# Kernel optimization log

Measured on AMD Instinct MI355X. Metric: run time of the kernel, lower is better.

The kernel has to match this reference:

```python
import jax, jax.numpy as jnp
import numpy as np

D_IN, D_K, D_V = 768, 128, 768


def setup_inputs() -> dict:
    key = jax.random.key(0)
    ks = jax.random.split(key, 7)
    x = jax.random.normal(ks[0], (4, 2048, D_IN), dtype=jnp.float32)
    s_in = 1.0 / np.sqrt(D_IN)
    Wq = jax.random.uniform(ks[1], (D_IN, D_K), minval=-s_in, maxval=s_in, dtype=jnp.float32)
    bq = jax.random.uniform(ks[2], (D_K,), minval=-s_in, maxval=s_in, dtype=jnp.float32)
    Wk = jax.random.uniform(ks[3], (D_IN, D_K), minval=-s_in, maxval=s_in, dtype=jnp.float32)
    bk = jax.random.uniform(ks[4], (D_K,), minval=-s_in, maxval=s_in, dtype=jnp.float32)
    Wv = jax.random.uniform(ks[5], (D_IN, D_V), minval=-s_in, maxval=s_in, dtype=jnp.float32)
    bv = jax.random.uniform(ks[6], (D_V,), minval=-s_in, maxval=s_in, dtype=jnp.float32)
    return {"x": x, "Wq": Wq, "bq": bq, "Wk": Wk, "bk": bk, "Wv": Wv, "bv": bv}


def reference(x, Wq, bq, Wk, bk, Wv, bv):
    # q,k: [b,t,d_k]; v: [b,t,d_v]
    q = jnp.einsum('bti,ik->btk', x, Wq) + bq
    k = jnp.einsum('bti,ik->btk', x, Wk) + bk
    v = jnp.einsum('bti,iv->btv', x, Wv) + bv
    scale = 1.0 / jnp.sqrt(jnp.asarray(D_K, dtype=jnp.float32))
    scores = jnp.einsum('bqk,btk->bqt', q, k) * scale  # [b,t,t]
    attn = jax.nn.softmax(scores, axis=-1)
    return jnp.einsum('bqt,btv->bqv', attn, v)
```

## Files before the change

### kernel.cpp

```cpp
#include <hip/hip_runtime.h>
#include <stdint.h>

typedef unsigned short u16;
typedef __attribute__((ext_vector_type(8))) short short8;
typedef __attribute__((ext_vector_type(4))) float f32x4;

#define BATCH 4
#define SEQ   2048
#define DIN   768
#define DK    128
#define DV    768
#define MTOT  (BATCH*SEQ)
#define NQKV  1024

__device__ __forceinline__ u16 f2bf(float f) {
  union { float f; uint32_t u; } v; v.f = f;
  uint32_t r = v.u + 0x7FFFu + ((v.u >> 16) & 1u);
  return (u16)(r >> 16);
}
__device__ __forceinline__ float bf2f(u16 h) {
  union { uint32_t u; float f; } v; v.u = ((uint32_t)h) << 16;
  return v.f;
}

template<int N> __device__ __forceinline__ void wait_vmcnt() {
  if constexpr (N == 0) asm volatile("s_waitcnt vmcnt(0)" ::: "memory");
  else if constexpr (N == 5) asm volatile("s_waitcnt vmcnt(5)" ::: "memory");
  else if constexpr (N == 10) asm volatile("s_waitcnt vmcnt(10)" ::: "memory");
}

__global__ __launch_bounds__(256) void pack_all(
    const float* __restrict__ Wq, const float* __restrict__ bq,
    const float* __restrict__ Wk, const float* __restrict__ bk,
    const float* __restrict__ Wv, const float* __restrict__ bv,
    u16* __restrict__ WbT, float* __restrict__ biasP) {
  const float qs = 0.088388347648318447f;
  __shared__ u16 tile[64][72];
  int y = blockIdx.y;
  const float* W; u16* dst; int ldw, nb; float sc;
  if (y < 2)      { W = Wq; dst = WbT;                       ldw = DK; sc = qs;   nb = y;     }
  else if (y < 4) { W = Wk; dst = WbT + (size_t)DK * DIN;    ldw = DK; sc = 1.0f; nb = y - 2; }
  else            { W = Wv; dst = WbT + (size_t)2*DK * DIN;  ldw = DV; sc = 1.0f; nb = y - 4; }
  int i0 = blockIdx.x * 64;
  int n0 = nb * 64;
  int tid = threadIdx.x;
  if (blockIdx.x == 0 && y == 0) {
    for (int n = tid; n < NQKV; n += 256)
      biasP[n] = (n < DK) ? bq[n] * qs : (n < 2*DK ? bk[n - DK] : bv[n - 2*DK]);
  }
  int tr = tid >> 2;
  int tc = (tid & 3) * 16;
  const float* src = W + (size_t)(i0 + tr) * ldw + n0 + tc;
  u16 o[16];
#pragma unroll
  for (int u = 0; u < 16; u += 4) {
    float4 v = *(const float4*)(src + u);
    o[u] = f2bf(v.x * sc); o[u+1] = f2bf(v.y * sc); o[u+2] = f2bf(v.z * sc); o[u+3] = f2bf(v.w * sc);
  }
  *(uint4*)&tile[tr][tc]     = *(const uint4*)&o[0];
  *(uint4*)&tile[tr][tc + 8] = *(const uint4*)&o[8];
  __syncthreads();
  u16 tmp[16];
#pragma unroll
  for (int u = 0; u < 16; ++u) tmp[u] = tile[tc + u][tr];
  u16* d = dst + (size_t)(n0 + tr) * DIN + i0 + tc;
  *(uint4*)d       = *(const uint4*)&tmp[0];
  *(uint4*)(d + 8) = *(const uint4*)&tmp[8];
}

__global__ void convert_x(const float* __restrict__ x, u16* __restrict__ xb) {
  int i = (blockIdx.x * blockDim.x + threadIdx.x) * 4;
  float4 v = *(const float4*)(x + i);
  u16 o[4] = { f2bf(v.x), f2bf(v.y), f2bf(v.z), f2bf(v.w) };
  *(uint2*)(xb + i) = *(const uint2*)o;
}

__global__ __launch_bounds__(512, 4) void gemm_proj(
    const u16* __restrict__ A, const u16* __restrict__ BT,
    u16* __restrict__ C0, u16* __restrict__ C1,
    const float* __restrict__ bias)
{
  const int NJ = 2, CH = 4, gx = 64;
  __shared__ u16 As[2][128][64];
  __shared__ u16 Bs[2][NJ * 64][64];
  const int tid = threadIdx.x;
  const int l   = tid & 63;
  const int wid = tid >> 6;
  const int wm  = wid >> 2;
  const int wn  = wid & 3;

  const int nwg = gridDim.x;
  const int cpx = nwg >> 3;
  const int bid = blockIdx.x;
  const int wg  = (bid & 7) * cpx + (bid >> 3);
  const int by  = wg / gx;
  const int bx  = wg - by * gx;
  const int m0  = bx * 128;
  const int n0  = by * (NJ * 64);

  f32x4 acc[4][NJ] = {};
  const int lr = l >> 3;
  const int lc = ((l & 7) ^ lr) * 8;
  const int ca = wid * CH;

  auto STAGE = [&](int buf, int k0) {
#pragma unroll
    for (int i = 0; i < CH; ++i) {
      int c = ca + i;
      if (c < 16) {
        const u16* src = A + (size_t)(m0 + c * 8 + lr) * DIN + k0 + lc;
        __builtin_amdgcn_global_load_lds(
            (const __attribute__((address_space(1))) unsigned int*)src,
            (__attribute__((address_space(3))) unsigned int*)&As[buf][c * 8][0],
            16, 0, 0);
      } else {
        int cb = c - 16;
        const u16* src = BT + (size_t)(n0 + cb * 8 + lr) * DIN + k0 + lc;
        __builtin_amdgcn_global_load_lds(
            (const __attribute__((address_space(1))) unsigned int*)src,
            (__attribute__((address_space(3))) unsigned int*)&Bs[buf][cb * 8][0],
            16, 0, 0);
      }
    }
  };

  STAGE(0, 0);
  __syncthreads();
  int cur = 0;
  for (int k0 = 0; k0 < DIN; k0 += 64) {
    if (k0 + 64 < DIN) STAGE(cur ^ 1, k0 + 64);
#pragma unroll
    for (int ks = 0; ks < 2; ++ks) {
      short8 af[4], bg[NJ];
#pragma unroll
      for (int i = 0; i < 4; ++i) {
        int row  = wm * 64 + i * 16 + (l & 15);
        int slot = (ks * 4 + (l >> 4)) ^ (row & 7);
        af[i] = *(const short8*)&As[cur][row][slot * 8];
      }
#pragma unroll
      for (int j = 0; j < NJ; ++j) {
        int row  = wn * (NJ * 16) + j * 16 + (l & 15);
        int slot = (ks * 4 + (l >> 4)) ^ (row & 7);
        bg[j] = *(const short8*)&Bs[cur][row][slot * 8];
      }
#pragma unroll
      for (int i = 0; i < 4; ++i)
#pragma unroll
        for (int j = 0; j < NJ; ++j)
          acc[i][j] = __builtin_amdgcn_mfma_f32_16x16x32_bf16(af[i], bg[j], acc[i][j], 0, 0, 0);
    }
    __syncthreads();
    cur ^= 1;
  }

  const int rbase = (l >> 4) * 4;
  const int cl    = l & 15;
#pragma unroll
  for (int i = 0; i < 4; ++i) {
#pragma unroll
    for (int j = 0; j < NJ; ++j) {
      int col = n0 + wn * (NJ * 16) + j * 16 + cl;
      int row0 = m0 + wm * 64 + i * 16 + rbase;
      float bv_ = bias[col];
      if (n0 < 256) {
#pragma unroll
        for (int q = 0; q < 4; ++q)
          C0[(size_t)(row0 + q) * 256 + col] = f2bf(acc[i][j][q] + bv_);
      } else {
        int b = row0 >> 11, t = row0 & 2047;
        u16 o[4];
#pragma unroll
        for (int q = 0; q < 4; ++q) o[q] = f2bf(acc[i][j][q] + bv_);
        *(uint2*)&C1[((size_t)b * DV + (col - 256)) * SEQ + t] = *(const uint2*)o;
      }
    }
  }
}

__global__ __launch_bounds__(512, 2) void gemm_pv(
    const u16* __restrict__ P, const u16* __restrict__ vT,
    float* __restrict__ out)
{
  const int NJ = 3, CH = 5, gx = 16, gy = 4, NT = SEQ / 64;
  __shared__ u16 As[3][128][64];
  __shared__ u16 Bs[3][NJ * 64][64];
  const int tid = threadIdx.x;
  const int l   = tid & 63;
  const int wid = tid >> 6;
  const int wm  = wid >> 2;
  const int wn  = wid & 3;

  const int nwg = gridDim.x;
  const int cpx = nwg >> 3;
  const int bid = blockIdx.x;
  const int wg  = (bid & 7) * cpx + (bid >> 3);
  const int z   = wg / (gx * gy);
  const int rem = wg - z * gx * gy;
  const int by  = rem / gx;
  const int bx  = rem - by * gx;
  const int m0  = bx * 128;
  const int n0  = by * (NJ * 64);

  const u16* A  = P  + (size_t)z * SEQ * SEQ;
  const u16* BT = vT + (size_t)z * DV * SEQ;

  f32x4 acc[4][NJ] = {};
  f32x4 accO[4] = {};
  const short8 kOnes = {16256,16256,16256,16256,16256,16256,16256,16256};

  const int lr = l >> 3;
  const int lc = ((l & 7) ^ lr) * 8;
  const int ca = wid * CH;

  auto STAGE = [&](int buf, int k0) {
#pragma unroll
    for (int i = 0; i < CH; ++i) {
      int c = ca + i;
      if (c < 16) {
        const u16* src = A + (size_t)(m0 + c * 8 + lr) * SEQ + k0 + lc;
        __builtin_amdgcn_global_load_lds(
            (const __attribute__((address_space(1))) unsigned int*)src,
            (__attribute__((address_space(3))) unsigned int*)&As[buf][c * 8][0],
            16, 0, 0);
      } else {
        int cb = c - 16;
        const u16* src = BT + (size_t)(n0 + cb * 8 + lr) * SEQ + k0 + lc;
        __builtin_amdgcn_global_load_lds(
            (const __attribute__((address_space(1))) unsigned int*)src,
            (__attribute__((address_space(3))) unsigned int*)&Bs[buf][cb * 8][0],
            16, 0, 0);
      }
    }
  };

  auto COMPUTE = [&](int buf) {
#pragma unroll
    for (int ks = 0; ks < 2; ++ks) {
      short8 af[4], bg[NJ];
#pragma unroll
      for (int i = 0; i < 4; ++i) {
        int row  = wm * 64 + i * 16 + (l & 15);
        int slot = (ks * 4 + (l >> 4)) ^ (row & 7);
        af[i] = *(const short8*)&As[buf][row][slot * 8];
      }
#pragma unroll
      for (int j = 0; j < NJ; ++j) {
        int row  = wn * (NJ * 16) + j * 16 + (l & 15);
        int slot = (ks * 4 + (l >> 4)) ^ (row & 7);
        bg[j] = *(const short8*)&Bs[buf][row][slot * 8];
      }
#pragma unroll
      for (int i = 0; i < 4; ++i)
#pragma unroll
        for (int j = 0; j < NJ; ++j)
          acc[i][j] = __builtin_amdgcn_mfma_f32_16x16x32_bf16(af[i], bg[j], acc[i][j], 0, 0, 0);
#pragma unroll
      for (int i = 0; i < 4; ++i)
        accO[i] = __builtin_amdgcn_mfma_f32_16x16x32_bf16(af[i], kOnes, accO[i], 0, 0, 0);
    }
  };

  STAGE(0, 0);
  STAGE(1, 64);
  int cur = 0;
  for (int t = 0; t < NT - 1; ++t) {
    wait_vmcnt<CH>();
    __builtin_amdgcn_s_barrier();
    COMPUTE(cur);
    if (t + 2 < NT) STAGE(cur + 2 >= 3 ? cur - 1 : cur + 2, (t + 2) * 64);
    cur = (cur + 1 == 3) ? 0 : cur + 1;
  }
  wait_vmcnt<0>();
  __builtin_amdgcn_s_barrier();
  COMPUTE(cur);

  const int rbase = (l >> 4) * 4;
  const int cl    = l & 15;
#pragma unroll
  for (int i = 0; i < 4; ++i) {
    f32x4 rs;
#pragma unroll
    for (int q = 0; q < 4; ++q) rs[q] = 1.0f / accO[i][q];
#pragma unroll
    for (int j = 0; j < NJ; ++j) {
      int col  = n0 + wn * (NJ * 16) + j * 16 + cl;
      int row0 = m0 + wm * 64 + i * 16 + rbase;
#pragma unroll
      for (int q = 0; q < 4; ++q)
        out[(size_t)z * SEQ * DV + (size_t)(row0 + q) * DV + col] = acc[i][j][q] * rs[q];
    }
  }
}

__global__ __launch_bounds__(512, 4) void sgemm_exp(
    const u16* __restrict__ qk, u16* __restrict__ P)
{
  __shared__ u16 As[128][128];
  __shared__ u16 Bs[128][128];
  const int tid = threadIdx.x;
  const int l   = tid & 63;
  const int wid = tid >> 6;
  const int wm  = wid >> 2;
  const int wn  = wid & 3;

  const int nwg = gridDim.x;
  const int cpx = nwg >> 3;
  const int bid = blockIdx.x;
  const int wg  = (bid & 7) * cpx + (bid >> 3);
  const int z   = wg >> 8;
  const int rem = wg & 255;
  const int by  = rem >> 4;
  const int bx  = rem & 15;
  const int m0  = bx * 128;
  const int n0  = by * 128;

  const u16* A  = qk + (size_t)z * SEQ * 256;
  const u16* BT = qk + DK + (size_t)z * SEQ * 256;

  const int rin  = l >> 4;
  const int s16  = l & 15;
#pragma unroll
  for (int i = 0; i < 8; ++i) {
    int c = wid * 8 + i;
    if (c < 32) {
      int r = c * 4 + rin;
      int gs = s16 ^ (r & 7);
      const u16* src = A + (size_t)(m0 + r) * 256 + gs * 8;
      __builtin_amdgcn_global_load_lds(
          (const __attribute__((address_space(1))) unsigned int*)src,
          (__attribute__((address_space(3))) unsigned int*)&As[c * 4][0],
          16, 0, 0);
    } else {
      int cb = c - 32;
      int r = cb * 4 + rin;
      int gs = s16 ^ (r & 7);
      const u16* src = BT + (size_t)(n0 + r) * 256 + gs * 8;
      __builtin_amdgcn_global_load_lds(
          (const __attribute__((address_space(1))) unsigned int*)src,
          (__attribute__((address_space(3))) unsigned int*)&Bs[cb * 4][0],
          16, 0, 0);
    }
  }
  __syncthreads();

  f32x4 acc[4][2] = {};
#pragma unroll
  for (int ks = 0; ks < 4; ++ks) {
    short8 af[4], bg[2];
#pragma unroll
    for (int i = 0; i < 4; ++i) {
      int row  = wm * 64 + i * 16 + (l & 15);
      int slot = (ks * 4 + (l >> 4)) ^ (row & 7);
      af[i] = *(const short8*)&As[row][slot * 8];
    }
#pragma unroll
    for (int j = 0; j < 2; ++j) {
      int row  = wn * 32 + j * 16 + (l & 15);
      int slot = (ks * 4 + (l >> 4)) ^ (row & 7);
      bg[j] = *(const short8*)&Bs[row][slot * 8];
    }
#pragma unroll
    for (int i = 0; i < 4; ++i)
#pragma unroll
      for (int j = 0; j < 2; ++j)
        acc[i][j] = __builtin_amdgcn_mfma_f32_16x16x32_bf16(af[i], bg[j], acc[i][j], 0, 0, 0);
  }

  const int rbase = (l >> 4) * 4;
  const int cl    = l & 15;
  u16* Pz = P + (size_t)z * SEQ * SEQ;
#pragma unroll
  for (int i = 0; i < 4; ++i)
#pragma unroll
    for (int j = 0; j < 2; ++j) {
      int col  = n0 + wn * 32 + j * 16 + cl;
      int row0 = m0 + wm * 64 + i * 16 + rbase;
#pragma unroll
      for (int q = 0; q < 4; ++q)
        Pz[(size_t)(row0 + q) * SEQ + col] = f2bf(__expf(acc[i][j][q]));
    }
}

extern "C" void kernel_launch(void* const* d_in, const int* in_sizes, int n_in,
                              void* d_out, int out_size, void* d_ws, size_t ws_size,
                              hipStream_t stream) {
  const float* x  = (const float*)d_in[0];
  const float* Wq = (const float*)d_in[1];
  const float* bq = (const float*)d_in[2];
  const float* Wk = (const float*)d_in[3];
  const float* bk = (const float*)d_in[4];
  const float* Wv = (const float*)d_in[5];
  const float* bv = (const float*)d_in[6];
  float* out = (float*)d_out;

  size_t off = 0;
  auto alloc = [&](size_t bytes) -> void* {
    void* p = (char*)d_ws + off;
    off += (bytes + 255) & ~(size_t)255;
    return p;
  };
  u16*   xb    = (u16*)alloc((size_t)MTOT * DIN * 2);
  u16*   WbT   = (u16*)alloc((size_t)NQKV * DIN * 2);
  float* biasP = (float*)alloc(NQKV * 4);
  u16*   qk    = (u16*)alloc((size_t)MTOT * 256 * 2);
  u16*   vT    = (u16*)alloc((size_t)BATCH * DV * SEQ * 2);
  u16*   P     = (u16*)alloc((size_t)BATCH * SEQ * SEQ * 2);
  if (off > ws_size) return;

  pack_all<<<dim3(DIN/64, 16), dim3(256), 0, stream>>>(Wq, bq, Wk, bk, Wv, bv, WbT, biasP);
  convert_x<<<dim3((MTOT * DIN / 4) / 256), dim3(256), 0, stream>>>(x, xb);

  gemm_proj<<<dim3(64 * 8), dim3(512), 0, stream>>>(xb, WbT, qk, vT, biasP);

  sgemm_exp<<<dim3(16 * 16 * BATCH), dim3(512), 0, stream>>>(qk, P);

  gemm_pv<<<dim3(16 * 4 * BATCH), dim3(512), 0, stream>>>(P, vT, out);
}
```

Measured before the change: 85.52 us.

## Merge prep kernels and interleave prefetch with MFMA in PV gemm

Combines the weight-packing and x-conversion kernels into one launch, removing one kernel launch and its gap. In the PV gemm, the global-to-LDS prefetch for tile t+2 is split across the two k-substeps and issued before the MFMAs, with s_setprio raised around the MFMA block, so loads overlap compute instead of following it. The loop is also unified so the last iteration needs no separate tail. It adds branching in the staging loop and changes instruction scheduling, which the compiler may not handle well.

```diff
diff --git a/kernel.cpp b/kernel.cpp
--- a/kernel.cpp
+++ b/kernel.cpp
@@ -18,10 +18,6 @@
   uint32_t r = v.u + 0x7FFFu + ((v.u >> 16) & 1u);
   return (u16)(r >> 16);
 }
-__device__ __forceinline__ float bf2f(u16 h) {
-  union { uint32_t u; float f; } v; v.u = ((uint32_t)h) << 16;
-  return v.f;
-}
 
 template<int N> __device__ __forceinline__ void wait_vmcnt() {
   if constexpr (N == 0) asm volatile("s_waitcnt vmcnt(0)" ::: "memory");
@@ -29,22 +25,32 @@
   else if constexpr (N == 10) asm volatile("s_waitcnt vmcnt(10)" ::: "memory");
 }
 
-__global__ __launch_bounds__(256) void pack_all(
+__global__ __launch_bounds__(256) void prep(
+    const float* __restrict__ x, u16* __restrict__ xb,
     const float* __restrict__ Wq, const float* __restrict__ bq,
     const float* __restrict__ Wk, const float* __restrict__ bk,
     const float* __restrict__ Wv, const float* __restrict__ bv,
     u16* __restrict__ WbT, float* __restrict__ biasP) {
   const float qs = 0.088388347648318447f;
   __shared__ u16 tile[64][72];
-  int y = blockIdx.y;
+  int b = blockIdx.x;
+  int tid = threadIdx.x;
+  if (b < 6144) {
+    int i = (b * 256 + tid) * 4;
+    float4 v = *(const float4*)(x + i);
+    u16 o[4] = { f2bf(v.x), f2bf(v.y), f2bf(v.z), f2bf(v.w) };
+    *(uint2*)(xb + i) = *(const uint2*)o;
+    return;
+  }
+  int bid2 = b - 6144;
+  int y   = bid2 / 12;
+  int i0  = (bid2 - y * 12) * 64;
   const float* W; u16* dst; int ldw, nb; float sc;
-  if (y < 2)      { W = Wq; dst = WbT;                       ldw = DK; sc = qs;   nb = y;     }
-  else if (y < 4) { W = Wk; dst = WbT + (size_t)DK * DIN;    ldw = DK; sc = 1.0f; nb = y - 2; }
-  else            { W = Wv; dst = WbT + (size_t)2*DK * DIN;  ldw = DV; sc = 1.0f; nb = y - 4; }
-  int i0 = blockIdx.x * 64;
+  if (y < 2)      { W = Wq; dst = WbT;                      ldw = DK; sc = qs;   nb = y;     }
+  else if (y < 4) { W = Wk; dst = WbT + (size_t)DK * DIN;   ldw = DK; sc = 1.0f; nb = y - 2; }
+  else            { W = Wv; dst = WbT + (size_t)2*DK * DIN; ldw = DV; sc = 1.0f; nb = y - 4; }
   int n0 = nb * 64;
-  int tid = threadIdx.x;
-  if (blockIdx.x == 0 && y == 0) {
+  if (i0 == 0 && y == 0) {
     for (int n = tid; n < NQKV; n += 256)
       biasP[n] = (n < DK) ? bq[n] * qs : (n < 2*DK ? bk[n - DK] : bv[n - 2*DK]);
   }
@@ -66,13 +72,6 @@
   u16* d = dst + (size_t)(n0 + tr) * DIN + i0 + tc;
   *(uint4*)d       = *(const uint4*)&tmp[0];
   *(uint4*)(d + 8) = *(const uint4*)&tmp[8];
-}
-
-__global__ void convert_x(const float* __restrict__ x, u16* __restrict__ xb) {
-  int i = (blockIdx.x * blockDim.x + threadIdx.x) * 4;
-  float4 v = *(const float4*)(x + i);
-  u16 o[4] = { f2bf(v.x), f2bf(v.y), f2bf(v.z), f2bf(v.w) };
-  *(uint2*)(xb + i) = *(const uint2*)o;
 }
 
 __global__ __launch_bounds__(512, 4) void gemm_proj(
@@ -213,9 +212,10 @@
   const int lc = ((l & 7) ^ lr) * 8;
   const int ca = wid * CH;
 
-  auto STAGE = [&](int buf, int k0) {
+  auto STAGE = [&](int buf, int k0, int i0, int i1) {
 #pragma unroll
     for (int i = 0; i < CH; ++i) {
+      if (i < i0 || i >= i1) continue;
       int c = ca + i;
       if (c < 16) {
         const u16* src = A + (size_t)(m0 + c * 8 + lr) * SEQ + k0 + lc;
@@ -234,7 +234,14 @@
     }
   };
 
-  auto COMPUTE = [&](int buf) {
+  STAGE(0, 0, 0, CH);
+  STAGE(1, 64, 0, CH);
+  int cur = 0;
+  for (int t = 0; t < NT; ++t) {
+    if (t == NT - 1) wait_vmcnt<0>(); else wait_vmcnt<CH>();
+    __builtin_amdgcn_s_barrier();
+    const int nxt2 = (cur + 2 >= 3) ? cur - 1 : cur + 2;
+    const bool pf = (t + 2 < NT);
 #pragma unroll
     for (int ks = 0; ks < 2; ++ks) {
       short8 af[4], bg[NJ];
@@ -242,38 +249,30 @@
       for (int i = 0; i < 4; ++i) {
         int row  = wm * 64 + i * 16 + (l & 15);
         int slot = (ks * 4 + (l >> 4)) ^ (row & 7);
-        af[i] = *(const short8*)&As[buf][row][slot * 8];
+        af[i] = *(const short8*)&As[cur][row][slot * 8];
       }
 #pragma unroll
       for (int j = 0; j < NJ; ++j) {
         int row  = wn * (NJ * 16) + j * 16 + (l & 15);
         int slot = (ks * 4 + (l >> 4)) ^ (row & 7);
-        bg[j] = *(const short8*)&Bs[buf][row][slot * 8];
-      }
-#pragma unroll
-      for (int i = 0; i < 4; ++i)
+        bg[j] = *(const short8*)&Bs[cur][row][slot * 8];
+      }
+      if (pf) {
+        if (ks == 0) STAGE(nxt2, (t + 2) * 64, 0, 3);
+        else         STAGE(nxt2, (t + 2) * 64, 3, CH);
+      }
+      __builtin_amdgcn_s_setprio(1);
+#pragma unroll
+      for (int i = 0; i < 4; ++i) {
 #pragma unroll
         for (int j = 0; j < NJ; ++j)
           acc[i][j] = __builtin_amdgcn_mfma_f32_16x16x32_bf16(af[i], bg[j], acc[i][j], 0, 0, 0);
-#pragma unroll
-      for (int i = 0; i < 4; ++i)
         accO[i] = __builtin_amdgcn_mfma_f32_16x16x32_bf16(af[i], kOnes, accO[i], 0, 0, 0);
-    }
-  };
-
-  STAGE(0, 0);
-  STAGE(1, 64);
-  int cur = 0;
-  for (int t = 0; t < NT - 1; ++t) {
-    wait_vmcnt<CH>();
-    __builtin_amdgcn_s_barrier();
-    COMPUTE(cur);
-    if (t + 2 < NT) STAGE(cur + 2 >= 3 ? cur - 1 : cur + 2, (t + 2) * 64);
+      }
+      __builtin_amdgcn_s_setprio(0);
+    }
     cur = (cur + 1 == 3) ? 0 : cur + 1;
   }
-  wait_vmcnt<0>();
-  __builtin_amdgcn_s_barrier();
-  COMPUTE(cur);
 
   const int rbase = (l >> 4) * 4;
   const int cl    = l & 15;
@@ -408,8 +407,7 @@
   u16*   P     = (u16*)alloc((size_t)BATCH * SEQ * SEQ * 2);
   if (off > ws_size) return;
 
-  pack_all<<<dim3(DIN/64, 16), dim3(256), 0, stream>>>(Wq, bq, Wk, bk, Wv, bv, WbT, biasP);
-  convert_x<<<dim3((MTOT * DIN / 4) / 256), dim3(256), 0, stream>>>(x, xb);
+  prep<<<dim3(6144 + 192), dim3(256), 0, stream>>>(x, xb, Wq, bq, Wk, bk, Wv, bv, WbT, biasP);
 
   gemm_proj<<<dim3(64 * 8), dim3(512), 0, stream>>>(xb, WbT, qk, vT, biasP);
 
```

Result: no change. 84.45 us (-1.3%).
